# Performance work log

Hardware: AMD Instinct MI355X
Metric: run time of the kernel (lower is better)

Reference implementation:

```python
import jax, jax.numpy as jnp
import numpy as np

N_NODES = 50000
N_EDGES = 800000   # avg degree ~16
IN_CH = 128
HID = 64


def setup_inputs() -> dict:
    key = jax.random.key(0)
    k0, k1, k2, k3 = jax.random.split(key, 4)
    x = jax.random.normal(k0, (N_NODES, IN_CH), dtype=jnp.float32)
    edge_index = jax.random.randint(k1, (2, N_EDGES), 0, N_NODES, dtype=jnp.int32)
    # Glorot-ish init like torch GCNConv
    W1 = jax.random.normal(k2, (IN_CH, HID), dtype=jnp.float32) / np.sqrt(IN_CH).astype(np.float32)
    b1 = jnp.zeros((HID,), dtype=jnp.float32)
    W2 = jax.random.normal(k3, (HID, HID), dtype=jnp.float32) / np.sqrt(HID).astype(np.float32)
    b2 = jnpp = jnp.zeros((HID,), dtype=jnp.float32)
    return {"x": x, "edge_index": edge_index, "W1": W1, "b1": b1, "W2": W2, "b2": b2}


def gcn_conv(x, src, dst, W, b, n):
    """GCNConv with self-loops already appended to (src, dst).
    out = D^{-1/2} (A + I) D^{-1/2} (x @ W) + b, symmetric normalization."""
    h = x @ W                                        # [N, out]
    deg = jax.ops.segment_sum(jnp.ones(src.shape, jnp.float32), dst, num_segments=n)
    dinv = jax.lax.rsqrt(jnp.maximum(deg, 1.0))      # deg >= 1 due to self-loops
    norm = dinv[src] * dinv[dst]                     # [E+N]
    msg = h[src] * norm[:, None]                     # gather + scale
    return jax.ops.segment_sum(msg, dst, num_segments=n) + b


def reference(x, edge_index, W1, b1, W2, b2):
    n = x.shape[0]
    loop = jnp.arange(n, dtype=edge_index.dtype)
    src = jnp.concatenate([edge_index[0], loop])     # add self-loops
    dst = jnp.concatenate([edge_index[1], loop])
    # encode: GCNConv -> ReLU -> GCNConv
    z = jax.nn.relu(gcn_conv(x, src, dst, W1, b1, n))
    z = gcn_conv(z, src, dst, W2, b2, n)
    # decode: gather endpoint embeddings, elementwise product, reduce over hidden
    return (z[edge_index[0]] * z[edge_index[1]]).sum(axis=1)   # [E]
```

## Files before the change

### kernel.cpp

```cpp
#include <hip/hip_runtime.h>
#include <hip/hip_fp16.h>

#define INCH 128
#define HIDC 64
#define CAP  64

typedef int            v4i __attribute__((ext_vector_type(4)));
typedef float          v4f __attribute__((ext_vector_type(4)));
typedef unsigned int   v4u __attribute__((ext_vector_type(4)));

__device__ inline float2 u2f(unsigned int u) {
    return __half22float2(__builtin_bit_cast(__half2, u));
}
__device__ inline unsigned int f2u(float a, float b) {
    __half2 h = __float22half2_rn(make_float2(a, b));
    return __builtin_bit_cast(unsigned int, h);
}

__global__ __launch_bounds__(128, 2) void build_gemm1_kernel(const int* __restrict__ src,
                                                             const int* __restrict__ dst,
                                                             int* __restrict__ count,
                                                             unsigned short* __restrict__ col,
                                                             const float* __restrict__ x,
                                                             const float* __restrict__ W,
                                                             __half* __restrict__ hs,
                                                             int E, int N, int GB) {
    int b = (int)blockIdx.x;
    if (b >= GB) {
        int eb = b - GB;
        int g = eb & 7;
        int chunkBase = (eb >> 3) * 2048;
        int t = (int)threadIdx.x;
        if (chunkBase + 2048 <= E) {
            v4i s4[4], d4[4];
            #pragma unroll
            for (int i = 0; i < 4; ++i) {
                int e0 = chunkBase + (i * 128 + t) * 4;
                d4[i] = *(const v4i*)(dst + e0);
                s4[i] = *(const v4i*)(src + e0);
            }
            #pragma unroll
            for (int i = 0; i < 4; ++i) {
                #pragma unroll
                for (int k = 0; k < 4; ++k) {
                    int d = d4[i][k];
                    if ((d & 7) == g) {
                        int r = atomicAdd(&count[d], 1);
                        if (r < CAP) col[(size_t)d * CAP + r] = (unsigned short)s4[i][k];
                    }
                }
            }
        } else {
            #pragma unroll
            for (int i = 0; i < 4; ++i) {
                int e0 = chunkBase + (i * 128 + t) * 4;
                for (int e = e0; e < e0 + 4 && e < E; ++e) {
                    int d = dst[e];
                    if ((d & 7) == g) {
                        int r = atomicAdd(&count[d], 1);
                        if (r < CAP) col[(size_t)d * CAP + r] = (unsigned short)src[e];
                    }
                }
            }
        }
    } else {
        int node = (b >> 1) * 128 + (int)threadIdx.x;
        int ch0 = (b & 1) * 32;
        if (node >= N) return;
        const float4* xr = (const float4*)(x + (size_t)node * INCH);
        float acc[32];
        #pragma unroll
        for (int c = 0; c < 32; ++c) acc[c] = 0.f;
        for (int kc = 0; kc < INCH / 4; ++kc) {
            float4 xk = xr[kc];
            const float* wr = W + (kc * 4) * HIDC + ch0;
            #pragma unroll
            for (int ch = 0; ch < 32; ++ch) acc[ch] = fmaf(xk.x, wr[ch], acc[ch]);
            #pragma unroll
            for (int ch = 0; ch < 32; ++ch) acc[ch] = fmaf(xk.y, wr[HIDC + ch], acc[ch]);
            #pragma unroll
            for (int ch = 0; ch < 32; ++ch) acc[ch] = fmaf(xk.z, wr[2 * HIDC + ch], acc[ch]);
            #pragma unroll
            for (int ch = 0; ch < 32; ++ch) acc[ch] = fmaf(xk.w, wr[3 * HIDC + ch], acc[ch]);
        }
        v4u hv[4];
        #pragma unroll
        for (int k = 0; k < 4; ++k) {
            #pragma unroll
            for (int e = 0; e < 4; ++e) {
                int c2 = k * 4 + e;
                hv[k][e] = f2u(acc[2 * c2], acc[2 * c2 + 1]);
            }
        }
        v4u* hr = (v4u*)(hs + (size_t)node * HIDC + ch0);
        #pragma unroll
        for (int k = 0; k < 4; ++k) hr[k] = hv[k];
    }
}

__global__ __launch_bounds__(256) void scale_kernel(const int* __restrict__ count,
                                                    __half* __restrict__ hs, int N) {
    int idx = (int)blockIdx.x * 256 + threadIdx.x;
    if (idx >= N * 8) return;
    int node = idx >> 3;
    float dn = rsqrtf((float)count[node] + 1.0f);
    v4u v = ((const v4u*)hs)[idx];
    v4u o;
    #pragma unroll
    for (int k = 0; k < 4; ++k) {
        float2 f = u2f(v[k]);
        o[k] = f2u(dn * f.x, dn * f.y);
    }
    ((v4u*)hs)[idx] = o;
}

__global__ __launch_bounds__(256) void agg1_gemm2_kernel(const int* __restrict__ count,
                                                         const unsigned short* __restrict__ col,
                                                         const __half* __restrict__ hs,
                                                         const float* __restrict__ b1,
                                                         const float* __restrict__ W2,
                                                         __half* __restrict__ out, int N) {
    __shared__ float sW2[HIDC * HIDC];
    __shared__ float sAgg[8 * HIDC];
    int t = (int)threadIdx.x;
    {
        const float4* w4 = (const float4*)W2;
        float4* s4 = (float4*)sW2;
        #pragma unroll
        for (int i = 0; i < 4; ++i) s4[t + 256 * i] = w4[t + 256 * i];
    }
    __syncthreads();

    int nl = t >> 5;
    int node = (int)blockIdx.x * 8 + nl;
    int c2 = t & 31;
    if (node >= N) return;
    int cnt = count[node];
    int deg = cnt < CAP ? cnt : CAP;
    const unsigned int* h2p = (const unsigned int*)hs;
    float2 acc = u2f(h2p[(size_t)node * 32 + c2]);
    const unsigned short* row = col + (size_t)node * CAP;
    for (int jb = 0; jb < deg; jb += 16) {
        int s[16];
        unsigned int v[16];
        #pragma unroll
        for (int u = 0; u < 16; ++u) {
            int idx = jb + u;
            s[u] = row[idx < deg ? idx : jb];
        }
        #pragma unroll
        for (int u = 0; u < 16; ++u)
            v[u] = h2p[(size_t)s[u] * 32 + c2];
        #pragma unroll
        for (int u = 0; u < 16; ++u) {
            if (jb + u < deg) {
                float2 f = u2f(v[u]);
                acc.x += f.x; acc.y += f.y;
            }
        }
    }
    float dn = rsqrtf((float)cnt + 1.0f);
    float2 bb = *(const float2*)(b1 + c2 * 2);
    float px = fmaxf(fmaf(acc.x, dn, bb.x), 0.f);
    float py = fmaxf(fmaf(acc.y, dn, bb.y), 0.f);
    ((float2*)sAgg)[nl * 32 + c2] = make_float2(px, py);
    __asm__ volatile("s_waitcnt lgkmcnt(0)" ::: "memory");

    float o0 = 0.f, o1 = 0.f;
    const float4* aF4 = (const float4*)(sAgg + nl * HIDC);
    #pragma unroll
    for (int kk = 0; kk < 16; ++kk) {
        float4 a4 = aF4[kk];
        float2 w0 = ((const float2*)(sW2 + (kk * 4 + 0) * HIDC))[c2];
        float2 w1 = ((const float2*)(sW2 + (kk * 4 + 1) * HIDC))[c2];
        float2 w2 = ((const float2*)(sW2 + (kk * 4 + 2) * HIDC))[c2];
        float2 w3 = ((const float2*)(sW2 + (kk * 4 + 3) * HIDC))[c2];
        o0 = fmaf(a4.x, w0.x, o0); o1 = fmaf(a4.x, w0.y, o1);
        o0 = fmaf(a4.y, w1.x, o0); o1 = fmaf(a4.y, w1.y, o1);
        o0 = fmaf(a4.z, w2.x, o0); o1 = fmaf(a4.z, w2.y, o1);
        o0 = fmaf(a4.w, w3.x, o0); o1 = fmaf(a4.w, w3.y, o1);
    }
    ((unsigned int*)out)[(size_t)node * 32 + c2] = f2u(o0 * dn, o1 * dn);
}

__global__ __launch_bounds__(256) void aggregate_kernel(const int* __restrict__ count,
                                                        const unsigned short* __restrict__ col,
                                                        const __half* __restrict__ hs,
                                                        const float* __restrict__ bias,
                                                        __half* __restrict__ agg, int N) {
    int node = blockIdx.x * 8 + (threadIdx.x >> 5);
    int c2 = threadIdx.x & 31;
    if (node >= N) return;
    int cnt = count[node];
    int deg = cnt < CAP ? cnt : CAP;
    const unsigned int* h2p = (const unsigned int*)hs;
    float2 acc = u2f(h2p[(size_t)node * 32 + c2]);
    const unsigned short* row = col + (size_t)node * CAP;
    for (int jb = 0; jb < deg; jb += 16) {
        int s[16];
        unsigned int v[16];
        #pragma unroll
        for (int u = 0; u < 16; ++u) {
            int idx = jb + u;
            s[u] = row[idx < deg ? idx : jb];
        }
        #pragma unroll
        for (int u = 0; u < 16; ++u)
            v[u] = h2p[(size_t)s[u] * 32 + c2];
        #pragma unroll
        for (int u = 0; u < 16; ++u) {
            if (jb + u < deg) {
                float2 f = u2f(v[u]);
                acc.x += f.x; acc.y += f.y;
            }
        }
    }
    float dn = rsqrtf((float)cnt + 1.0f);
    float2 bb = *(const float2*)(bias + c2 * 2);
    ((unsigned int*)agg)[(size_t)node * 32 + c2] =
        f2u(fmaf(acc.x, dn, bb.x), fmaf(acc.y, dn, bb.y));
}

__global__ __launch_bounds__(256) void decode_kernel(const int* __restrict__ src,
                                                     const int* __restrict__ dst,
                                                     const __half* __restrict__ z,
                                                     float* __restrict__ out, int E) {
    long long tid = (long long)blockIdx.x * 256 + threadIdx.x;
    int g = (int)(tid >> 3);
    int q = threadIdx.x & 7;
    int e0 = g * 4;
    if (e0 >= E) return;
    const v4u* z8 = (const v4u*)z;
    bool full = (e0 + 3 < E);
    int s[4], d[4];
    if (full) {
        v4i sv = __builtin_nontemporal_load((const v4i*)(src + e0));
        v4i dv = __builtin_nontemporal_load((const v4i*)(dst + e0));
        s[0]=sv.x; s[1]=sv.y; s[2]=sv.z; s[3]=sv.w;
        d[0]=dv.x; d[1]=dv.y; d[2]=dv.z; d[3]=dv.w;
    } else {
        #pragma unroll
        for (int k = 0; k < 4; ++k) {
            int e = e0 + k < E ? e0 + k : e0;
            s[k] = src[e]; d[k] = dst[e];
        }
    }
    v4u a[4], b[4];
    #pragma unroll
    for (int k = 0; k < 4; ++k) a[k] = z8[(size_t)s[k] * 8 + q];
    #pragma unroll
    for (int k = 0; k < 4; ++k) b[k] = z8[(size_t)d[k] * 8 + q];
    float p[4];
    #pragma unroll
    for (int k = 0; k < 4; ++k) {
        float acc = 0.f;
        #pragma unroll
        for (int j = 0; j < 4; ++j) {
            float2 fa = u2f(a[k][j]);
            float2 fb = u2f(b[k][j]);
            acc = fmaf(fa.x, fb.x, acc);
            acc = fmaf(fa.y, fb.y, acc);
        }
        p[k] = acc;
    }
    #pragma unroll
    for (int m = 4; m; m >>= 1) {
        #pragma unroll
        for (int k = 0; k < 4; ++k) p[k] += __shfl_xor(p[k], m, 64);
    }
    if (q == 0) {
        if (full) {
            v4f r; r.x = p[0]; r.y = p[1]; r.z = p[2]; r.w = p[3];
            __builtin_nontemporal_store(r, (v4f*)(out + e0));
        } else {
            for (int k = 0; k < 4 && e0 + k < E; ++k) out[e0 + k] = p[k];
        }
    }
}

extern "C" void kernel_launch(void* const* d_in, const int* in_sizes, int n_in,
                              void* d_out, int out_size, void* d_ws, size_t ws_size,
                              hipStream_t stream) {
    const float* x  = (const float*)d_in[0];
    const int*   ei = (const int*)d_in[1];
    const float* W1 = (const float*)d_in[2];
    const float* b1 = (const float*)d_in[3];
    const float* W2 = (const float*)d_in[4];
    const float* b2 = (const float*)d_in[5];
    float* out = (float*)d_out;

    const int hid  = in_sizes[3];
    const int inch = in_sizes[2] / hid;
    const int N    = in_sizes[0] / inch;
    const int E    = in_sizes[1] / 2;
    const int* srcp = ei;
    const int* dstp = ei + E;

    char* p = (char*)d_ws;
    auto alloc = [&](size_t bytes) { char* r = p; p += (bytes + 255) & ~(size_t)255; return r; };
    int*            count = (int*)alloc((size_t)N * 4);
    unsigned short* col   = (unsigned short*)alloc((size_t)N * CAP * 2);
    __half*         h1s   = (__half*)alloc((size_t)N * HIDC * 2);
    __half*         h2s   = (__half*)alloc((size_t)N * HIDC * 2);
    __half*         zt    = (__half*)alloc((size_t)N * HIDC * 2);

    (void)hipMemsetAsync(count, 0, (size_t)N * 4, stream);

    int GB  = 2 * ((N + 127) / 128);
    int EBK = 8 * ((E + 2047) / 2048);
    build_gemm1_kernel<<<GB + EBK, 128, 0, stream>>>(srcp, dstp, count, col,
                                                     x, W1, h1s, E, N, GB);
    scale_kernel<<<(N * 8 + 255) / 256, 256, 0, stream>>>(count, h1s, N);

    agg1_gemm2_kernel<<<(N + 7) / 8, 256, 0, stream>>>(count, col, h1s, b1, W2, h2s, N);

    aggregate_kernel<<<(N + 7) / 8, 256, 0, stream>>>(count, col, h2s, b2, zt, N);

    long long groups = ((long long)E + 3) / 4;
    long long blocksD = (groups * 8 + 255) / 256;
    decode_kernel<<<(int)blocksD, 256, 0, stream>>>(srcp, dstp, zt, out, E);
}
```

Before: 197.1 us.

## Fold source-degree scaling into aggregation, drop scale kernel, widen decode per thread

Removes the separate scale kernel and instead applies each neighbor's rsqrt(deg) weight inside the aggregation loops, which adds an extra gathered count load per neighbor. The agg1_gemm2 output is no longer pre-scaled by dn. The edge-build pass now partitions destinations by (d>>4)&7 instead of d&7, which changes how atomics to count are spread across blocks. The decode kernel processes 8 edges per thread group instead of 4, giving more loads in flight at the cost of more registers.

```diff
diff --git a/kernel.cpp b/kernel.cpp
--- a/kernel.cpp
+++ b/kernel.cpp
@@ -44,7 +44,7 @@
                 #pragma unroll
                 for (int k = 0; k < 4; ++k) {
                     int d = d4[i][k];
-                    if ((d & 7) == g) {
+                    if (((d >> 4) & 7) == g) {
                         int r = atomicAdd(&count[d], 1);
                         if (r < CAP) col[(size_t)d * CAP + r] = (unsigned short)s4[i][k];
                     }
@@ -56,7 +56,7 @@
                 int e0 = chunkBase + (i * 128 + t) * 4;
                 for (int e = e0; e < e0 + 4 && e < E; ++e) {
                     int d = dst[e];
-                    if ((d & 7) == g) {
+                    if (((d >> 4) & 7) == g) {
                         int r = atomicAdd(&count[d], 1);
                         if (r < CAP) col[(size_t)d * CAP + r] = (unsigned short)src[e];
                     }
@@ -96,22 +96,6 @@
         #pragma unroll
         for (int k = 0; k < 4; ++k) hr[k] = hv[k];
     }
-}
-
-__global__ __launch_bounds__(256) void scale_kernel(const int* __restrict__ count,
-                                                    __half* __restrict__ hs, int N) {
-    int idx = (int)blockIdx.x * 256 + threadIdx.x;
-    if (idx >= N * 8) return;
-    int node = idx >> 3;
-    float dn = rsqrtf((float)count[node] + 1.0f);
-    v4u v = ((const v4u*)hs)[idx];
-    v4u o;
-    #pragma unroll
-    for (int k = 0; k < 4; ++k) {
-        float2 f = u2f(v[k]);
-        o[k] = f2u(dn * f.x, dn * f.y);
-    }
-    ((v4u*)hs)[idx] = o;
 }
 
 __global__ __launch_bounds__(256) void agg1_gemm2_kernel(const int* __restrict__ count,
@@ -137,12 +121,15 @@
     if (node >= N) return;
     int cnt = count[node];
     int deg = cnt < CAP ? cnt : CAP;
+    float dn = rsqrtf((float)cnt + 1.0f);
     const unsigned int* h2p = (const unsigned int*)hs;
-    float2 acc = u2f(h2p[(size_t)node * 32 + c2]);
+    float2 self = u2f(h2p[(size_t)node * 32 + c2]);
+    float2 acc = make_float2(self.x * dn, self.y * dn);
     const unsigned short* row = col + (size_t)node * CAP;
     for (int jb = 0; jb < deg; jb += 16) {
         int s[16];
         unsigned int v[16];
+        int cv[16];
         #pragma unroll
         for (int u = 0; u < 16; ++u) {
             int idx = jb + u;
@@ -152,14 +139,18 @@
         for (int u = 0; u < 16; ++u)
             v[u] = h2p[(size_t)s[u] * 32 + c2];
         #pragma unroll
+        for (int u = 0; u < 16; ++u)
+            cv[u] = count[s[u]];
+        #pragma unroll
         for (int u = 0; u < 16; ++u) {
             if (jb + u < deg) {
                 float2 f = u2f(v[u]);
-                acc.x += f.x; acc.y += f.y;
-            }
-        }
-    }
-    float dn = rsqrtf((float)cnt + 1.0f);
+                float w = rsqrtf((float)cv[u] + 1.0f);
+                acc.x = fmaf(f.x, w, acc.x);
+                acc.y = fmaf(f.y, w, acc.y);
+            }
+        }
+    }
     float2 bb = *(const float2*)(b1 + c2 * 2);
     float px = fmaxf(fmaf(acc.x, dn, bb.x), 0.f);
     float py = fmaxf(fmaf(acc.y, dn, bb.y), 0.f);
@@ -180,7 +171,7 @@
         o0 = fmaf(a4.z, w2.x, o0); o1 = fmaf(a4.z, w2.y, o1);
         o0 = fmaf(a4.w, w3.x, o0); o1 = fmaf(a4.w, w3.y, o1);
     }
-    ((unsigned int*)out)[(size_t)node * 32 + c2] = f2u(o0 * dn, o1 * dn);
+    ((unsigned int*)out)[(size_t)node * 32 + c2] = f2u(o0, o1);
 }
 
 __global__ __launch_bounds__(256) void aggregate_kernel(const int* __restrict__ count,
@@ -193,12 +184,15 @@
     if (node >= N) return;
     int cnt = count[node];
     int deg = cnt < CAP ? cnt : CAP;
+    float dn = rsqrtf((float)cnt + 1.0f);
     const unsigned int* h2p = (const unsigned int*)hs;
-    float2 acc = u2f(h2p[(size_t)node * 32 + c2]);
+    float2 self = u2f(h2p[(size_t)node * 32 + c2]);
+    float2 acc = make_float2(self.x * dn, self.y * dn);
     const unsigned short* row = col + (size_t)node * CAP;
     for (int jb = 0; jb < deg; jb += 16) {
         int s[16];
         unsigned int v[16];
+        int cv[16];
         #pragma unroll
         for (int u = 0; u < 16; ++u) {
             int idx = jb + u;
@@ -208,14 +202,18 @@
         for (int u = 0; u < 16; ++u)
             v[u] = h2p[(size_t)s[u] * 32 + c2];
         #pragma unroll
+        for (int u = 0; u < 16; ++u)
+            cv[u] = count[s[u]];
+        #pragma unroll
         for (int u = 0; u < 16; ++u) {
             if (jb + u < deg) {
                 float2 f = u2f(v[u]);
-                acc.x += f.x; acc.y += f.y;
-            }
-        }
-    }
-    float dn = rsqrtf((float)cnt + 1.0f);
+                float w = rsqrtf((float)cv[u] + 1.0f);
+                acc.x = fmaf(f.x, w, acc.x);
+                acc.y = fmaf(f.y, w, acc.y);
+            }
+        }
+    }
     float2 bb = *(const float2*)(bias + c2 * 2);
     ((unsigned int*)agg)[(size_t)node * 32 + c2] =
         f2u(fmaf(acc.x, dn, bb.x), fmaf(acc.y, dn, bb.y));
@@ -228,31 +226,35 @@
     long long tid = (long long)blockIdx.x * 256 + threadIdx.x;
     int g = (int)(tid >> 3);
     int q = threadIdx.x & 7;
-    int e0 = g * 4;
+    int e0 = g * 8;
     if (e0 >= E) return;
     const v4u* z8 = (const v4u*)z;
-    bool full = (e0 + 3 < E);
-    int s[4], d[4];
+    bool full = (e0 + 7 < E);
+    int s[8], d[8];
     if (full) {
-        v4i sv = __builtin_nontemporal_load((const v4i*)(src + e0));
-        v4i dv = __builtin_nontemporal_load((const v4i*)(dst + e0));
-        s[0]=sv.x; s[1]=sv.y; s[2]=sv.z; s[3]=sv.w;
-        d[0]=dv.x; d[1]=dv.y; d[2]=dv.z; d[3]=dv.w;
+        v4i sv0 = __builtin_nontemporal_load((const v4i*)(src + e0));
+        v4i sv1 = __builtin_nontemporal_load((const v4i*)(src + e0 + 4));
+        v4i dv0 = __builtin_nontemporal_load((const v4i*)(dst + e0));
+        v4i dv1 = __builtin_nontemporal_load((const v4i*)(dst + e0 + 4));
+        s[0]=sv0.x; s[1]=sv0.y; s[2]=sv0.z; s[3]=sv0.w;
+        s[4]=sv1.x; s[5]=sv1.y; s[6]=sv1.z; s[7]=sv1.w;
+        d[0]=dv0.x; d[1]=dv0.y; d[2]=dv0.z; d[3]=dv0.w;
+        d[4]=dv1.x; d[5]=dv1.y; d[6]=dv1.z; d[7]=dv1.w;
     } else {
         #pragma unroll
-        for (int k = 0; k < 4; ++k) {
+        for (int k = 0; k < 8; ++k) {
             int e = e0 + k < E ? e0 + k : e0;
             s[k] = src[e]; d[k] = dst[e];
         }
     }
-    v4u a[4], b[4];
-    #pragma unroll
-    for (int k = 0; k < 4; ++k) a[k] = z8[(size_t)s[k] * 8 + q];
-    #pragma unroll
-    for (int k = 0; k < 4; ++k) b[k] = z8[(size_t)d[k] * 8 + q];
-    float p[4];
-    #pragma unroll
-    for (int k = 0; k < 4; ++k) {
+    v4u a[8], b[8];
+    #pragma unroll
+    for (int k = 0; k < 8; ++k) a[k] = z8[(size_t)s[k] * 8 + q];
+    #pragma unroll
+    for (int k = 0; k < 8; ++k) b[k] = z8[(size_t)d[k] * 8 + q];
+    float p[8];
+    #pragma unroll
+    for (int k = 0; k < 8; ++k) {
         float acc = 0.f;
         #pragma unroll
         for (int j = 0; j < 4; ++j) {
@@ -266,14 +268,16 @@
     #pragma unroll
     for (int m = 4; m; m >>= 1) {
         #pragma unroll
-        for (int k = 0; k < 4; ++k) p[k] += __shfl_xor(p[k], m, 64);
+        for (int k = 0; k < 8; ++k) p[k] += __shfl_xor(p[k], m, 64);
     }
     if (q == 0) {
         if (full) {
-            v4f r; r.x = p[0]; r.y = p[1]; r.z = p[2]; r.w = p[3];
-            __builtin_nontemporal_store(r, (v4f*)(out + e0));
+            v4f r0; r0.x = p[0]; r0.y = p[1]; r0.z = p[2]; r0.w = p[3];
+            v4f r1; r1.x = p[4]; r1.y = p[5]; r1.z = p[6]; r1.w = p[7];
+            __builtin_nontemporal_store(r0, (v4f*)(out + e0));
+            __builtin_nontemporal_store(r1, (v4f*)(out + e0 + 4));
         } else {
-            for (int k = 0; k < 4 && e0 + k < E; ++k) out[e0 + k] = p[k];
+            for (int k = 0; k < 8 && e0 + k < E; ++k) out[e0 + k] = p[k];
         }
     }
 }
@@ -310,13 +314,12 @@
     int EBK = 8 * ((E + 2047) / 2048);
     build_gemm1_kernel<<<GB + EBK, 128, 0, stream>>>(srcp, dstp, count, col,
                                                      x, W1, h1s, E, N, GB);
-    scale_kernel<<<(N * 8 + 255) / 256, 256, 0, stream>>>(count, h1s, N);
 
     agg1_gemm2_kernel<<<(N + 7) / 8, 256, 0, stream>>>(count, col, h1s, b1, W2, h2s, N);
 
     aggregate_kernel<<<(N + 7) / 8, 256, 0, stream>>>(count, col, h2s, b2, zt, N);
 
-    long long groups = ((long long)E + 3) / 4;
+    long long groups = ((long long)E + 7) / 8;
     long long blocksD = (groups * 8 + 255) / 256;
     decode_kernel<<<(int)blocksD, 256, 0, stream>>>(srcp, dstp, zt, out, E);
 }
```

Result: no change. 198.0 us (+0.5%).
